# Performance work log

Measured on AMD Instinct MI355X. Metric: run time of the kernel, lower is better.

## Reference

```python
import jax, jax.numpy as jnp
import numpy as np

LAMBDA_SMOOTHNESS = 1.0
NUM_NODES = 100000
NUM_EDGES = 320000
D_FEAT = 256
NUM_GRAPHS = 128
NUM_CLASSES = 10


def setup_inputs() -> dict:
    key = jax.random.key(0)
    k1, k2, k3, k4, k5 = jax.random.split(key, 5)
    logits = jax.random.normal(k1, (NUM_GRAPHS, NUM_CLASSES), dtype=jnp.float32)
    labels = jax.random.randint(k2, (NUM_GRAPHS,), 0, NUM_CLASSES, dtype=jnp.int64)
    x = jax.random.normal(k3, (NUM_NODES, D_FEAT), dtype=jnp.float32)
    edge_index = jax.random.randint(k4, (2, NUM_EDGES), 0, NUM_NODES, dtype=jnp.int64)
    batch = jnp.sort(jax.random.randint(k5, (NUM_NODES,), 0, NUM_GRAPHS, dtype=jnp.int64))
    return {"logits": logits, "labels": labels, "x": x,
            "edge_index": edge_index, "batch": batch}


def reference(logits, labels, x, edge_index, batch):
    # --- cross entropy over graphs (mean reduction, like F.cross_entropy) ---
    logp = jax.nn.log_softmax(logits, axis=-1)
    ce_loss = -jnp.mean(jnp.take_along_axis(logp, labels[:, None], axis=1))

    # --- Dirichlet smoothness energy, vectorized over all graphs ---
    num_graphs = (jnp.max(batch) + 1).astype(x.dtype)
    row, col = edge_index[0], edge_index[1]
    # edges crossing graph boundaries are dropped by the per-graph edge_mask
    within = (batch[row] == batch[col]).astype(x.dtype)  # [E]
    # per-node degree counting only within-graph edges (== per-graph degree)
    deg = jax.ops.segment_sum(within, row, num_segments=x.shape[0])  # [N]
    deg_inv_sqrt = jnp.where(deg > 0, deg ** -0.5, jnp.zeros_like(deg))
    norm = deg_inv_sqrt[row] * deg_inv_sqrt[col] * within  # [E]
    diff = x[row] - x[col]  # [E, D]
    energy = jnp.sum(norm * jnp.sum(diff * diff, axis=-1))
    smoothness_loss = energy / num_graphs

    return ce_loss + LAMBDA_SMOOTHNESS * smoothness_loss
```

## Files before the change

### kernel.cpp

```cpp
#include <hip/hip_runtime.h>
#include <math.h>

__global__ void ce_kernel(const float* __restrict__ logits,
                          const int* __restrict__ labels,
                          double* __restrict__ ce_out, int G, int C) {
    __shared__ float sh[128];
    int g = threadIdx.x;
    float lp = 0.f;
    if (g < G) {
        const float* lg = logits + (size_t)g * C;
        float m = lg[0];
        for (int d = 1; d < C; ++d) m = fmaxf(m, lg[d]);
        float s = 0.f;
        for (int d = 0; d < C; ++d) s += expf(lg[d] - m);
        lp = lg[labels[g]] - m - logf(s);
    }
    sh[threadIdx.x] = lp;
    __syncthreads();
    for (int o = blockDim.x / 2; o > 0; o >>= 1) {
        if (threadIdx.x < o) sh[threadIdx.x] += sh[threadIdx.x + o];
        __syncthreads();
    }
    if (threadIdx.x == 0) *ce_out = -(double)sh[0] / (double)G;
}

__global__ void deg_kernel(const int* __restrict__ row,
                           const int* __restrict__ col,
                           const int* __restrict__ batch,
                           unsigned int* __restrict__ deg, int E) {
    int e = blockIdx.x * blockDim.x + threadIdx.x;
    if (e >= E) return;
    int r = row[e], c = col[e];
    if (batch[r] == batch[c]) atomicAdd(&deg[r], 1u);
}

__global__ void energy_kernel(const float* __restrict__ x,
                              const int* __restrict__ row,
                              const int* __restrict__ col,
                              const int* __restrict__ batch,
                              const unsigned int* __restrict__ deg,
                              double* __restrict__ energy_acc,
                              int E, int D4 ) {
    int gtid = blockIdx.x * blockDim.x + threadIdx.x;
    int wave = gtid >> 6;
    int lane = threadIdx.x & 63;

    int e = wave * 64 + lane;
    int r = 0, c = 0;
    float norm = 0.f;
    bool hit = false;
    if (e < E) {
        r = row[e];
        c = col[e];
        if (batch[r] == batch[c]) {
            unsigned int dr = deg[r], dc = deg[c];
            if (dr > 0 && dc > 0) {
                float ir = 1.0f / sqrtf((float)dr);
                float ic = 1.0f / sqrtf((float)dc);
                norm = ir * ic;
                hit = true;
            }
        }
    }

    double wsum = 0.0;
    unsigned long long mask = __ballot(hit);
    while (mask) {
        int src = __ffsll((unsigned long long)mask) - 1;
        mask &= mask - 1;
        int rr = __shfl(r, src);
        int cc = __shfl(c, src);
        float nn = __shfl(norm, src);
        const float4 a = ((const float4*)(x + (size_t)rr * (size_t)(D4 * 4)))[lane];
        const float4 b = ((const float4*)(x + (size_t)cc * (size_t)(D4 * 4)))[lane];
        float dx = a.x - b.x, dy = a.y - b.y, dz = a.z - b.z, dw = a.w - b.w;
        float ss = dx * dx + dy * dy + dz * dz + dw * dw;
        #pragma unroll
        for (int o = 32; o > 0; o >>= 1) ss += __shfl_xor(ss, o);
        if (lane == 0) wsum += (double)(nn * ss);
    }
    if (lane == 0 && wsum != 0.0) atomicAdd(energy_acc, wsum);
}

__global__ void finalize_kernel(const double* __restrict__ ce,
                                const double* __restrict__ energy,
                                const int* __restrict__ batch,
                                int N, float* __restrict__ out) {
    if (threadIdx.x == 0 && blockIdx.x == 0) {
        double num_graphs = (double)(batch[N - 1] + 1);
        out[0] = (float)(*ce + *energy / num_graphs);
    }
}

extern "C" void kernel_launch(void* const* d_in, const int* in_sizes, int n_in,
                              void* d_out, int out_size, void* d_ws, size_t ws_size,
                              hipStream_t stream) {
    const float* logits = (const float*)d_in[0];
    const int* labels = (const int*)d_in[1];
    const float* x = (const float*)d_in[2];
    const int* edge_index = (const int*)d_in[3];
    const int* batch = (const int*)d_in[4];

    const int C = 10;
    const int G = in_sizes[0] / C;
    const int E = in_sizes[3] / 2;
    const int N = in_sizes[4];
    const int D = in_sizes[2] / N;
    const int D4 = D / 4;

    const int* row = edge_index;
    const int* col = edge_index + E;

    size_t degBytes = ((size_t)N * 4 + 15) & ~(size_t)15;
    unsigned int* deg = (unsigned int*)d_ws;
    double* energy_acc = (double*)((char*)d_ws + degBytes);
    double* ce_acc = (double*)((char*)d_ws + degBytes + 8);

    hipMemsetAsync(d_ws, 0, degBytes + 16, stream);

    ce_kernel<<<1, 128, 0, stream>>>(logits, labels, ce_acc, G, C);

    int degBlocks = (E + 255) / 256;
    deg_kernel<<<degBlocks, 256, 0, stream>>>(row, col, batch, deg, E);

    int waves = (E + 63) / 64;
    int eBlocks = (waves + 3) / 4;
    energy_kernel<<<eBlocks, 256, 0, stream>>>(x, row, col, batch, deg,
                                               energy_acc, E, D4);

    finalize_kernel<<<1, 64, 0, stream>>>(ce_acc, energy_acc, batch, N,
                                          (float*)d_out);
}
```

Measured before the change: 23.68 us.

## Compact within-graph edges and fuse CE and finalize into fewer kernels

The degree kernel now also appends within-graph edge pairs to a compacted list via an atomic counter and computes the cross-entropy in block 0. The energy kernel then iterates only over the compacted hits with a fixed grid and finalizes the output via a last-block-done counter. The memset is replaced by an init kernel. The aim is to avoid rescanning all edges in the energy pass and to cut launch count, at the cost of atomic contention for compaction and a grid-wide completion counter.

```diff
diff --git a/kernel.cpp b/kernel.cpp
--- a/kernel.cpp
+++ b/kernel.cpp
@@ -1,94 +1,97 @@
 #include <hip/hip_runtime.h>
 #include <math.h>
 
-__global__ void ce_kernel(const float* __restrict__ logits,
-                          const int* __restrict__ labels,
-                          double* __restrict__ ce_out, int G, int C) {
-    __shared__ float sh[128];
-    int g = threadIdx.x;
-    float lp = 0.f;
-    if (g < G) {
-        const float* lg = logits + (size_t)g * C;
-        float m = lg[0];
-        for (int d = 1; d < C; ++d) m = fmaxf(m, lg[d]);
-        float s = 0.f;
-        for (int d = 0; d < C; ++d) s += expf(lg[d] - m);
-        lp = lg[labels[g]] - m - logf(s);
-    }
-    sh[threadIdx.x] = lp;
-    __syncthreads();
-    for (int o = blockDim.x / 2; o > 0; o >>= 1) {
-        if (threadIdx.x < o) sh[threadIdx.x] += sh[threadIdx.x + o];
-        __syncthreads();
-    }
-    if (threadIdx.x == 0) *ce_out = -(double)sh[0] / (double)G;
+__global__ void k1_init(unsigned int* __restrict__ deg, int N,
+                        double* __restrict__ energy_acc,
+                        unsigned int* __restrict__ hitCount,
+                        unsigned int* __restrict__ doneCount) {
+    int tid = blockIdx.x * blockDim.x + threadIdx.x;
+    int nthreads = gridDim.x * blockDim.x;
+    for (int i = tid; i < N; i += nthreads) deg[i] = 0u;
+    if (tid == 0) { *energy_acc = 0.0; *hitCount = 0u; *doneCount = 0u; }
 }
 
-__global__ void deg_kernel(const int* __restrict__ row,
-                           const int* __restrict__ col,
-                           const int* __restrict__ batch,
-                           unsigned int* __restrict__ deg, int E) {
+__global__ __launch_bounds__(256) void k2_deg_compact_ce(
+        const int* __restrict__ row, const int* __restrict__ col,
+        const int* __restrict__ batch, unsigned int* __restrict__ deg,
+        unsigned int* __restrict__ hitCount, int2* __restrict__ hits, int E,
+        const float* __restrict__ logits, const int* __restrict__ labels,
+        double* __restrict__ ce_acc, int G, int C) {
     int e = blockIdx.x * blockDim.x + threadIdx.x;
-    if (e >= E) return;
-    int r = row[e], c = col[e];
-    if (batch[r] == batch[c]) atomicAdd(&deg[r], 1u);
+    if (e < E) {
+        int r = row[e], c = col[e];
+        if (batch[r] == batch[c]) {
+            atomicAdd(&deg[r], 1u);
+            unsigned int idx = atomicAdd(hitCount, 1u);
+            hits[idx] = make_int2(r, c);
+        }
+    }
+    if (blockIdx.x == 0) {
+        __shared__ float sh[128];
+        int g = threadIdx.x;
+        if (g < 128) {
+            float lp = 0.f;
+            if (g < G) {
+                const float* lg = logits + (size_t)g * C;
+                float m = lg[0];
+                for (int d = 1; d < C; ++d) m = fmaxf(m, lg[d]);
+                float s = 0.f;
+                for (int d = 0; d < C; ++d) s += expf(lg[d] - m);
+                lp = lg[labels[g]] - m - logf(s);
+            }
+            sh[g] = lp;
+        }
+        __syncthreads();
+        for (int o = 64; o > 0; o >>= 1) {
+            if (threadIdx.x < o) sh[threadIdx.x] += sh[threadIdx.x + o];
+            __syncthreads();
+        }
+        if (threadIdx.x == 0) *ce_acc = -(double)sh[0] / (double)G;
+    }
 }
 
-__global__ void energy_kernel(const float* __restrict__ x,
-                              const int* __restrict__ row,
-                              const int* __restrict__ col,
-                              const int* __restrict__ batch,
-                              const unsigned int* __restrict__ deg,
-                              double* __restrict__ energy_acc,
-                              int E, int D4 ) {
-    int gtid = blockIdx.x * blockDim.x + threadIdx.x;
-    int wave = gtid >> 6;
-    int lane = threadIdx.x & 63;
-
-    int e = wave * 64 + lane;
-    int r = 0, c = 0;
-    float norm = 0.f;
-    bool hit = false;
-    if (e < E) {
-        r = row[e];
-        c = col[e];
-        if (batch[r] == batch[c]) {
-            unsigned int dr = deg[r], dc = deg[c];
-            if (dr > 0 && dc > 0) {
-                float ir = 1.0f / sqrtf((float)dr);
-                float ic = 1.0f / sqrtf((float)dc);
-                norm = ir * ic;
-                hit = true;
-            }
-        }
-    }
+__global__ __launch_bounds__(256) void k3_energy_finalize(
+        const float* __restrict__ x, const unsigned int* __restrict__ deg,
+        const unsigned int* __restrict__ hitCount, const int2* __restrict__ hits,
+        double* __restrict__ energy_acc, unsigned int* __restrict__ doneCount,
+        const double* __restrict__ ce_acc, const int* __restrict__ batch,
+        int N, int D, float* __restrict__ out) {
+    const int tid = blockIdx.x * blockDim.x + threadIdx.x;
+    const int lane = threadIdx.x & 63;
+    const int wave = tid >> 6;
+    const int nwaves = (gridDim.x * blockDim.x) >> 6;
+    const int nH = (int)(*hitCount);
 
     double wsum = 0.0;
-    unsigned long long mask = __ballot(hit);
-    while (mask) {
-        int src = __ffsll((unsigned long long)mask) - 1;
-        mask &= mask - 1;
-        int rr = __shfl(r, src);
-        int cc = __shfl(c, src);
-        float nn = __shfl(norm, src);
-        const float4 a = ((const float4*)(x + (size_t)rr * (size_t)(D4 * 4)))[lane];
-        const float4 b = ((const float4*)(x + (size_t)cc * (size_t)(D4 * 4)))[lane];
+    for (int h = wave; h < nH; h += nwaves) {
+        int2 rc = hits[h];
+        unsigned int dr = deg[rc.x];
+        unsigned int dc = deg[rc.y];
+        if (dc == 0u) continue;
+        const float4 a = ((const float4*)(x + (size_t)rc.x * (size_t)D))[lane];
+        const float4 b = ((const float4*)(x + (size_t)rc.y * (size_t)D))[lane];
         float dx = a.x - b.x, dy = a.y - b.y, dz = a.z - b.z, dw = a.w - b.w;
         float ss = dx * dx + dy * dy + dz * dz + dw * dw;
         #pragma unroll
         for (int o = 32; o > 0; o >>= 1) ss += __shfl_xor(ss, o);
-        if (lane == 0) wsum += (double)(nn * ss);
+        if (lane == 0) {
+            float ir = 1.0f / sqrtf((float)dr);
+            float ic = 1.0f / sqrtf((float)dc);
+            wsum += (double)((ir * ic) * ss);
+        }
     }
     if (lane == 0 && wsum != 0.0) atomicAdd(energy_acc, wsum);
-}
 
-__global__ void finalize_kernel(const double* __restrict__ ce,
-                                const double* __restrict__ energy,
-                                const int* __restrict__ batch,
-                                int N, float* __restrict__ out) {
-    if (threadIdx.x == 0 && blockIdx.x == 0) {
-        double num_graphs = (double)(batch[N - 1] + 1);
-        out[0] = (float)(*ce + *energy / num_graphs);
+    __syncthreads();
+    if (threadIdx.x == 0) {
+        __threadfence();
+        unsigned int done = atomicAdd(doneCount, 1u);
+        if (done == gridDim.x - 1) {
+            double energy = atomicAdd(energy_acc, 0.0);
+            double ce = *ce_acc;
+            double ng = (double)(batch[N - 1] + 1);
+            out[0] = (float)(ce + energy / ng);
+        }
     }
 }
 
@@ -106,28 +109,30 @@
     const int E = in_sizes[3] / 2;
     const int N = in_sizes[4];
     const int D = in_sizes[2] / N;
-    const int D4 = D / 4;
 
     const int* row = edge_index;
     const int* col = edge_index + E;
 
-    size_t degBytes = ((size_t)N * 4 + 15) & ~(size_t)15;
-    unsigned int* deg = (unsigned int*)d_ws;
-    double* energy_acc = (double*)((char*)d_ws + degBytes);
-    double* ce_acc = (double*)((char*)d_ws + degBytes + 8);
+    size_t off = 0;
+    unsigned int* deg = (unsigned int*)((char*)d_ws + off); off += (size_t)N * 4;
+    off = (off + 15) & ~(size_t)15;
+    double* energy_acc = (double*)((char*)d_ws + off);      off += 8;
+    double* ce_acc     = (double*)((char*)d_ws + off);      off += 8;
+    unsigned int* hitCount  = (unsigned int*)((char*)d_ws + off); off += 4;
+    unsigned int* doneCount = (unsigned int*)((char*)d_ws + off); off += 4;
+    off = (off + 15) & ~(size_t)15;
+    int2* hits = (int2*)((char*)d_ws + off);
 
-    hipMemsetAsync(d_ws, 0, degBytes + 16, stream);
+    float* out = (float*)d_out;
 
-    ce_kernel<<<1, 128, 0, stream>>>(logits, labels, ce_acc, G, C);
+    k1_init<<<256, 256, 0, stream>>>(deg, N, energy_acc, hitCount, doneCount);
 
-    int degBlocks = (E + 255) / 256;
-    deg_kernel<<<degBlocks, 256, 0, stream>>>(row, col, batch, deg, E);
+    int k2Blocks = (E + 255) / 256;
+    k2_deg_compact_ce<<<k2Blocks, 256, 0, stream>>>(
+        row, col, batch, deg, hitCount, hits, E,
+        logits, labels, ce_acc, G, C);
 
-    int waves = (E + 63) / 64;
-    int eBlocks = (waves + 3) / 4;
-    energy_kernel<<<eBlocks, 256, 0, stream>>>(x, row, col, batch, deg,
-                                               energy_acc, E, D4);
-
-    finalize_kernel<<<1, 64, 0, stream>>>(ce_acc, energy_acc, batch, N,
-                                          (float*)d_out);
+    k3_energy_finalize<<<128, 256, 0, stream>>>(
+        x, deg, hitCount, hits, energy_acc, doneCount,
+        ce_acc, batch, N, D, out);
 }
```

New measurement: 43.08 us. 1.82x slower.
